# Optimization experiments

Measured on AMD Instinct MI355X. Metric: run time of the kernel, lower is better.

The kernel has to match this reference:

```python
import jax, jax.numpy as jnp
import numpy as np

N, HID, NC, GD, HEADS = 8192, 768, 18, 256, 2
K = 5            # knn_k in the module
E_CLS = 324      # class co-occurrence edges (<= 18*18)
NEG_SLOPE = 0.2  # GATv2Conv default
EPS = 1e-5       # LayerNorm eps


def _ln(x, g, b):
    m = x.mean(-1, keepdims=True)
    v = ((x - m) ** 2).mean(-1, keepdims=True)
    return (x - m) / jnp.sqrt(v + EPS) * g + b


def _seg_softmax(scores, seg, n):
    # softmax over edges grouped by destination node (irregular segments)
    m = jax.ops.segment_max(scores, seg, num_segments=n)
    e = jnp.exp(scores - m[seg])
    s = jax.ops.segment_sum(e, seg, num_segments=n)
    return e / s[seg]


def _gatv2(x, src, dst, wl, bl, wr, br, att, bias, n):
    # PyG GATv2Conv (heads=2, concat=True), eval mode (dropout off)
    xl = (x @ wl.T + bl).reshape(n, HEADS, GD)   # lin_l -> source features
    xr = (x @ wr.T + br).reshape(n, HEADS, GD)   # lin_r -> target features
    h = jax.nn.leaky_relu(xl[src] + xr[dst], NEG_SLOPE)     # [E,H,D]
    scores = jnp.einsum('ehd,hd->eh', h, att)               # [E,H]
    alpha = _seg_softmax(scores, dst, n)
    out = jax.ops.segment_sum(xl[src] * alpha[..., None], dst, num_segments=n)
    return out.reshape(n, HEADS * GD) + bias


def _add_self_loops(src, dst, n):
    # GATv2Conv default add_self_loops=True
    loops = jnp.arange(n)
    return jnp.concatenate([src, loops]), jnp.concatenate([dst, loops])


def _knn_edges(x, k):
    # torch_cluster knn_graph(x, k, loop=True): self-distance 0 is always kept
    x2 = jnp.sum(x * x, -1)
    d = x2[:, None] + x2[None, :] - 2.0 * (x @ x.T)  # [N,N] sq. distances
    _, idx = jax.lax.top_k(-d, k)                    # k nearest incl. self
    src = idx.reshape(-1)                            # neighbors (sources)
    dst = jnp.repeat(jnp.arange(x.shape[0]), k)      # centers (targets)
    return src, dst


def _forward(class_edge_index, instance_features, class_emb,
             gc_wl, gc_bl, gc_wr, gc_br, gc_att, gc_bias,
             gi_wl, gi_bl, gi_wr, gi_br, gi_att, gi_bias,
             q_w, q_b, ctx_w, ctx_b, wv, bv, wo, bo, ln1_g, ln1_b,
             ln2_g, ln2_b, gw_w, gw_b, temperature):
    n = instance_features.shape[0]
    # class graph GATv2
    csrc, cdst = _add_self_loops(class_edge_index[0], class_edge_index[1], NC)
    class_feat = _gatv2(class_emb, csrc, cdst, gc_wl, gc_bl, gc_wr, gc_br,
                        gc_att, gc_bias, NC)                  # [NC, 512]
    # kNN graph + instance GATv2
    isrc, idst = _knn_edges(instance_features, K)
    isrc, idst = _add_self_loops(isrc, idst, n)
    gnn_inst = _gatv2(instance_features, isrc, idst, gi_wl, gi_bl, gi_wr,
                      gi_br, gi_att, gi_bias, n)              # [N, 512]
    ctx = class_feat.mean(0, keepdims=True) + gnn_inst        # [N, 512]
    # cross-attention fusion: q/k/v have seq_len 1, so softmax == 1 and the
    # MHA output reduces to out_proj(v_proj(context_proj(ctx))); query path
    # (q_w, q_b) cancels out of the forward value.
    ctx_p = ctx @ ctx_w.T + ctx_b                             # [N, 768]
    attn = (ctx_p @ wv.T + bv) @ wo.T + bo                    # [N, 768]
    fused = _ln(instance_features + attn, ln1_g, ln1_b)
    # pre_classifier: LayerNorm -> GELU (exact) -> Dropout(eval)
    pre = jax.nn.gelu(_ln(fused, ln2_g, ln2_b), approximate=False)
    # GroupWiseLinear
    logits = jnp.einsum('ch,nh->nc', gw_w[0], pre) + gw_b[0]
    return logits / temperature  # eval-mode temperature scaling


def setup_inputs() -> dict:
    key = jax.random.key(0)
    ks = jax.random.split(key, 32)
    rn = lambda i, shape, s: jax.random.normal(ks[i], shape, jnp.float32) * s
    inp = {
        'instance_features': jax.random.normal(ks[0], (N, HID), jnp.float32),
        'class_edge_index': jax.random.randint(ks[1], (2, E_CLS), 0, NC),
        'class_emb': rn(2, (NC, HID), 0.02),
        'gc_wl': rn(3, (HEADS * GD, HID), 0.02), 'gc_bl': jnp.zeros(HEADS * GD),
        'gc_wr': rn(4, (HEADS * GD, HID), 0.02), 'gc_br': jnp.zeros(HEADS * GD),
        'gc_att': rn(5, (HEADS, GD), 0.1), 'gc_bias': jnp.zeros(HEADS * GD),
        'gi_wl': rn(6, (HEADS * GD, HID), 0.02), 'gi_bl': jnp.zeros(HEADS * GD),
        'gi_wr': rn(7, (HEADS * GD, HID), 0.02), 'gi_br': jnp.zeros(HEADS * GD),
        'gi_att': rn(8, (HEADS, GD), 0.1), 'gi_bias': jnp.zeros(HEADS * GD),
        'q_w': rn(9, (HID, HID), 0.02), 'q_b': jnp.zeros(HID),
        'ctx_w': rn(10, (HID, HEADS * GD), 0.02), 'ctx_b': jnp.zeros(HID),
        'wv': rn(11, (HID, HID), 0.02), 'bv': jnp.zeros(HID),
        'wo': rn(12, (HID, HID), 0.02), 'bo': jnp.zeros(HID),
        'ln1_g': jnp.ones(HID), 'ln1_b': jnp.zeros(HID),
        'ln2_g': jnp.ones(HID), 'ln2_b': jnp.zeros(HID),
        'gw_w': rn(13, (1, NC, HID), 0.036), 'gw_b': jnp.zeros((1, NC)),
        'temperature': jnp.ones(1),
    }
    return inp


def reference(instance_features, class_edge_index, class_emb,
              gc_wl, gc_bl, gc_wr, gc_br, gc_att, gc_bias,
              gi_wl, gi_bl, gi_wr, gi_br, gi_att, gi_bias,
              q_w, q_b, ctx_w, ctx_b, wv, bv, wo, bo, ln1_g, ln1_b,
              ln2_g, ln2_b, gw_w, gw_b, temperature):
    return _forward(class_edge_index, instance_features, class_emb,
                    gc_wl, gc_bl, gc_wr, gc_br, gc_att, gc_bias,
                    gi_wl, gi_bl, gi_wr, gi_br, gi_att, gi_bias,
                    q_w, q_b, ctx_w, ctx_b, wv, bv, wo, bo, ln1_g, ln1_b,
                    ln2_g, ln2_b, gw_w, gw_b, temperature)
```

## Files before the change

kernel.cpp:

```cpp
#include <hip/hip_runtime.h>
#include <hip/hip_bf16.h>
#include <hip/hip_fp16.h>
#include <math.h>

#define NN 8192
#define HIDD 768
#define NCLS 18
#define OD 512
#define ETOT 342
#define NEG 0.2f
#define LN_EPS 1e-5f

typedef __attribute__((ext_vector_type(8))) short bf16x8;
typedef __attribute__((ext_vector_type(4))) float f32x4;

__device__ __forceinline__ void top5_insert(float s, int idx,
    float& d0, float& d1, float& d2, float& d3, float& d4,
    int& i0, int& i1, int& i2, int& i3, int& i4) {
  if (s >= d4) return;
  if (s < d3) {
    d4 = d3; i4 = i3;
    if (s < d2) {
      d3 = d2; i3 = i2;
      if (s < d1) {
        d2 = d1; i2 = i1;
        if (s < d0) { d1 = d0; i1 = i0; d0 = s; i0 = idx; }
        else        { d1 = s;  i1 = idx; }
      } else { d2 = s; i2 = idx; }
    } else { d3 = s; i3 = idx; }
  } else { d4 = s; i4 = idx; }
}

__device__ __forceinline__ void top8k_insert(unsigned key, unsigned (&kk)[8]) {
  if (key >= kk[7]) return;
  int rank = 0;
  #pragma unroll
  for (int k = 0; k < 7; ++k) rank += (key >= kk[k]) ? 1 : 0;
  #pragma unroll
  for (int k = 7; k >= 1; --k) if (k > rank) kk[k] = kk[k-1];
  #pragma unroll
  for (int k = 0; k < 8; ++k) if (k == rank) kk[k] = key;
}

__device__ __forceinline__ void stage16(const void* g, void* l) {
  __builtin_amdgcn_global_load_lds(
      (const __attribute__((address_space(1))) unsigned int*)g,
      (__attribute__((address_space(3))) unsigned int*)l, 16, 0, 0);
}

__device__ __forceinline__ ushort f2b(float v) {
  __hip_bfloat16 b = __float2bfloat16(v);
  return *(ushort*)&b;
}
__device__ __forceinline__ float b2f(ushort u) {
  unsigned uv = ((unsigned)u) << 16;
  return *(float*)&uv;
}

__global__ __launch_bounds__(256) void prep1_kernel(
    const float* __restrict__ X, ushort* __restrict__ Xh, float* __restrict__ x2,
    const float* __restrict__ gi_wl, const float* __restrict__ gi_wr,
    ushort* __restrict__ wlrh,
    const float* __restrict__ cemb, const float* __restrict__ gc_wl,
    const float* __restrict__ gc_bl, const float* __restrict__ gc_wr,
    const float* __restrict__ gc_br, float* __restrict__ xlc, float* __restrict__ xrc,
    const float* __restrict__ wv, const float* __restrict__ ctx_b,
    const float* __restrict__ bv, float* __restrict__ t1b,
    const float* __restrict__ gi_bl, const float* __restrict__ gi_br,
    float* __restrict__ bb) {
  const int bx = blockIdx.x, tid = threadIdx.x;
  if (bx < 2048) {
    const int row = bx * 4 + (tid >> 6);
    const int lane = tid & 63;
    const float4* src = (const float4*)(X + (size_t)row * HIDD);
    ushort4* dst = (ushort4*)(Xh + (size_t)row * HIDD);
    float s = 0.f;
    #pragma unroll
    for (int q = 0; q < 3; ++q) {
      float4 v = src[lane + q * 64];
      s += v.x * v.x + v.y * v.y + v.z * v.z + v.w * v.w;
      dst[lane + q * 64] = make_ushort4(f2b(v.x), f2b(v.y), f2b(v.z), f2b(v.w));
    }
    #pragma unroll
    for (int off = 32; off; off >>= 1) s += __shfl_down(s, off);
    if (lane == 0) x2[row] = s;
  } else if (bx < 2816) {
    int rel = bx - 2048;
    const float* src = gi_wl; ushort* dst = wlrh;
    if (rel >= 384) { rel -= 384; src = gi_wr; dst = wlrh + (size_t)OD * HIDD; }
    const int i = rel * 256 + tid;
    float4 v = ((const float4*)src)[i];
    ((ushort4*)dst)[i] = make_ushort4(f2b(v.x), f2b(v.y), f2b(v.z), f2b(v.w));
  } else if (bx < 2888) {
    int t = (bx - 2816) * 256 + tid;
    const float* W; const float* b; float* Y;
    if (t < NCLS * OD) { W = gc_wl; b = gc_bl; Y = xlc; }
    else { t -= NCLS * OD; W = gc_wr; b = gc_br; Y = xrc; }
    const int row = t / OD, o = t - row * OD;
    const float4* xr4 = (const float4*)(cemb + (size_t)row * HIDD);
    const float4* wr4 = (const float4*)(W + (size_t)o * HIDD);
    float acc = 0.f;
    for (int k = 0; k < HIDD / 4; ++k) {
      const float4 a = xr4[k], w4 = wr4[k];
      acc += a.x * w4.x + a.y * w4.y + a.z * w4.z + a.w * w4.w;
    }
    Y[t] = acc + b[o];
  } else if (bx < 2891) {
    const int t = (bx - 2888) * 256 + tid;
    if (t < HIDD) {
      const float4* cb4 = (const float4*)ctx_b;
      const float4* wv4 = (const float4*)(wv + (size_t)t * HIDD);
      float acc = 0.f;
      for (int k = 0; k < HIDD / 4; ++k) {
        const float4 a = cb4[k], w4 = wv4[k];
        acc += a.x * w4.x + a.y * w4.y + a.z * w4.z + a.w * w4.w;
      }
      t1b[t] = acc + bv[t];
    }
  } else {
    const int t = (bx - 2891) * 256 + tid;
    if (t < OD) bb[t] = gi_bl[t];
    else if (t < 2 * OD) bb[t] = gi_br[t - OD];
  }
}

__global__ __launch_bounds__(256) void gemm_nn_f32(const float* __restrict__ A,
    const float* __restrict__ B, float* __restrict__ Cf, ushort* __restrict__ Ch,
    int M, int N, int K) {
  __shared__ float As[64][33];
  __shared__ float Bs[32][65];
  const int tid = threadIdx.x, tx = tid & 15, ty = tid >> 4;
  const int r0 = blockIdx.x * 64, c0 = blockIdx.y * 64;
  float acc[4][4] = {};
  for (int kt = 0; kt < K; kt += 32) {
    __syncthreads();
    #pragma unroll
    for (int l = 0; l < 8; ++l) {
      const int idx = l * 256 + tid;
      const int m = idx >> 5, k = idx & 31;
      As[m][k] = A[(size_t)(r0 + m) * K + kt + k];
      const int k2 = idx >> 6, n = idx & 63;
      Bs[k2][n] = B[(size_t)(kt + k2) * N + c0 + n];
    }
    __syncthreads();
    #pragma unroll
    for (int k = 0; k < 32; ++k) {
      float a[4], b[4];
      #pragma unroll
      for (int i = 0; i < 4; ++i) a[i] = As[ty * 4 + i][k];
      #pragma unroll
      for (int j = 0; j < 4; ++j) b[j] = Bs[k][tx * 4 + j];
      #pragma unroll
      for (int i = 0; i < 4; ++i)
        #pragma unroll
        for (int j = 0; j < 4; ++j) acc[i][j] += a[i] * b[j];
    }
  }
  #pragma unroll
  for (int i = 0; i < 4; ++i) {
    const int r = r0 + ty * 4 + i;
    #pragma unroll
    for (int j = 0; j < 4; ++j) {
      const int c = c0 + tx * 4 + j;
      if (Ch) Ch[(size_t)r * N + c] = f2b(acc[i][j]);
      else    Cf[(size_t)r * N + c] = acc[i][j];
    }
  }
}

__global__ __launch_bounds__(256) void prep2_kernel(
    const float* __restrict__ wo, const float* __restrict__ t1b,
    const float* __restrict__ bo, float* __restrict__ bp,
    const int* __restrict__ cei, const float* __restrict__ xlc,
    const float* __restrict__ xrc, const float* __restrict__ gc_att,
    const float* __restrict__ gc_bias, float* __restrict__ cmean) {
  __shared__ float sc[ETOT * 2];
  __shared__ int es[ETOT], ed[ETOT];
  __shared__ float mx[NCLS][2], sm[NCLS][2];
  const int bx = blockIdx.x, tid = threadIdx.x;
  if (bx < 3) {
    const int t = bx * 256 + tid;
    if (t < HIDD) {
      const float4* tb4 = (const float4*)t1b;
      const float4* wo4 = (const float4*)(wo + (size_t)t * HIDD);
      float acc = 0.f;
      for (int k = 0; k < HIDD / 4; ++k) {
        const float4 a = tb4[k], w4 = wo4[k];
        acc += a.x * w4.x + a.y * w4.y + a.z * w4.z + a.w * w4.w;
      }
      bp[t] = acc + bo[t];
    }
  } else {
    for (int e = tid; e < ETOT; e += 256) {
      if (e < 324) { es[e] = cei[e]; ed[e] = cei[324 + e]; }
      else         { es[e] = e - 324; ed[e] = e - 324; }
    }
    __syncthreads();
    const int lane = tid & 63, w = tid >> 6;
    for (int t = w; t < ETOT * 2; t += 4) {
      const int e = t >> 1, h = t & 1;
      const float* xlr = xlc + (size_t)es[e] * OD + h * 256;
      const float* xrr = xrc + (size_t)ed[e] * OD + h * 256;
      const float* ar  = gc_att + h * 256;
      float s = 0.f;
      for (int d = lane; d < 256; d += 64) {
        float v = xlr[d] + xrr[d];
        v = v > 0.f ? v : NEG * v;
        s += v * ar[d];
      }
      #pragma unroll
      for (int off = 32; off; off >>= 1) s += __shfl_down(s, off);
      if (lane == 0) sc[t] = s;
    }
    __syncthreads();
    if (tid < NCLS * 2) {
      const int d = tid >> 1, h = tid & 1;
      float m = -3e38f;
      for (int e = 0; e < ETOT; ++e) if (ed[e] == d) m = fmaxf(m, sc[e * 2 + h]);
      float ssum = 0.f;
      for (int e = 0; e < ETOT; ++e) if (ed[e] == d) ssum += expf(sc[e * 2 + h] - m);
      mx[d][h] = m; sm[d][h] = 1.f / ssum;
    }
    __syncthreads();
    for (int t = tid; t < ETOT * 2; t += 256) {
      const int e = t >> 1, h = t & 1;
      sc[t] = expf(sc[t] - mx[ed[e]][h]) * sm[ed[e]][h];
    }
    __syncthreads();
    for (int c = tid; c < OD; c += 256) {
      const int h = c >> 8;
      float acc = 0.f;
      for (int e = 0; e < ETOT; ++e) acc += sc[e * 2 + h] * xlc[(size_t)es[e] * OD + c];
      cmean[c] = acc * (1.f / 18.f) + gc_bias[c];
    }
  }
}

__global__ __launch_bounds__(256, 4) void dist_sym_mfma(
    const ushort* __restrict__ Xh, const float* __restrict__ x2,
    unsigned* __restrict__ pck) {
  __shared__ __align__(16) char lds[32768];
  __shared__ float x2i[128], x2j[128];
  char* const sA = lds;
  char* const sB = lds + 16384;
  __half* const Dh = (__half*)lds;
  unsigned* const ck = (unsigned*)lds;

  const int t = blockIdx.x;
  int by = (int)((sqrtf(8.0f * (float)t + 1.0f) - 1.0f) * 0.5f);
  while ((by + 1) * (by + 2) / 2 <= t) ++by;
  while (by * (by + 1) / 2 > t) --by;
  const int bx = t - by * (by + 1) / 2;

  const int tid = threadIdx.x;
  const int lane = tid & 63, wid = tid >> 6;
  const int fr = lane & 15, fq = lane >> 4;
  const int i0 = bx * 128, j0 = by * 128;
  const int wr = (wid >> 1) * 64, wc = (wid & 1) * 64;
  const bool diag = (bx == by);

  if (tid < 128) x2i[tid] = x2[i0 + tid];
  else x2j[tid - 128] = x2[j0 + tid - 128];

  f32x4 acc[4][4] = {};
  for (int kt = 0; kt < HIDD; kt += 64) {
    __syncthreads();
    #pragma unroll
    for (int q = 0; q < 4; ++q) {
      const int chunkid = q * 256 + tid;
      const int row = chunkid >> 3, cc = chunkid & 7;
      const bf16x8 va = *(const bf16x8*)(Xh + (size_t)(i0 + row) * HIDD + kt + cc * 8);
      const bf16x8 vb = *(const bf16x8*)(Xh + (size_t)(j0 + row) * HIDD + kt + cc * 8);
      const int wi = row * 128 + ((cc ^ (row & 7)) << 4);
      *(bf16x8*)(sA + wi) = va;
      *(bf16x8*)(sB + wi) = vb;
    }
    __syncthreads();
    #pragma unroll
    for (int kk = 0; kk < 2; ++kk) {
      bf16x8 bh[4];
      #pragma unroll
      for (int n = 0; n < 4; ++n) {
        const int br = wc + n * 16 + fr;
        bh[n] = *(const bf16x8*)(sB + br * 128 + (((kk * 4 + fq) ^ (br & 7)) << 4));
      }
      #pragma unroll
      for (int m = 0; m < 4; ++m) {
        const int ar = wr + m * 16 + fr;
        const bf16x8 a = *(const bf16x8*)(sA + ar * 128 + (((kk * 4 + fq) ^ (ar & 7)) << 4));
        #pragma unroll
        for (int n = 0; n < 4; ++n)
          acc[m][n] = __builtin_amdgcn_mfma_f32_16x16x32_bf16(a, bh[n], acc[m][n], 0, 0, 0);
      }
    }
  }
  __syncthreads();
  #pragma unroll
  for (int n = 0; n < 4; ++n) {
    const int col = wc + n * 16 + fr;
    #pragma unroll
    for (int m = 0; m < 4; ++m) {
      #pragma unroll
      for (int j = 0; j < 4; ++j) {
        const int row = wr + m * 16 + fq * 4 + j;
        Dh[row * 128 + ((col + row) & 127)] = __float2half(-2.0f * acc[m][n][j]);
      }
    }
  }
  __syncthreads();

  unsigned ki[8], kj[8];
  #pragma unroll
  for (int k = 0; k < 8; ++k) { ki[k] = 0xFFFFFFFFu; kj[k] = 0xFFFFFFFFu; }
  const int r = tid & 127, h = tid >> 7;
  for (int c = 0; c < 64; ++c) {
    const int col = h * 64 + c;
    const float s = x2j[col] - 768.0f + __half2float(Dh[r * 128 + ((col + r) & 127)]);
    const ushort u = __half_as_ushort(__float2half(s));
    const ushort k16 = (u & 0x8000) ? (ushort)(~u) : (ushort)(u | 0x8000);
    top8k_insert(((unsigned)k16 << 16) | (unsigned)(j0 + col), ki);
  }
  if (!diag) {
    for (int c = 0; c < 64; ++c) {
      const int cr = h * 64 + c;
      const float s = x2i[cr] - 768.0f + __half2float(Dh[cr * 128 + ((r + cr) & 127)]);
      const ushort u = __half_as_ushort(__float2half(s));
      const ushort k16 = (u & 0x8000) ? (ushort)(~u) : (ushort)(u | 0x8000);
      top8k_insert(((unsigned)k16 << 16) | (unsigned)(i0 + cr), kj);
    }
  }
  __syncthreads();
  #pragma unroll
  for (int k = 0; k < 8; ++k) ck[tid * 8 + k] = ki[k];
  __syncthreads();
  if (tid < 128) {
    unsigned mk[8];
    #pragma unroll
    for (int k = 0; k < 8; ++k) mk[k] = ck[tid * 8 + k];
    #pragma unroll
    for (int k = 0; k < 8; ++k) top8k_insert(ck[(tid + 128) * 8 + k], mk);
    const size_t base = ((size_t)(i0 + tid) * 64 + by) * 8;
    #pragma unroll
    for (int k = 0; k < 8; ++k) pck[base + k] = mk[k];
  }
  if (!diag) {
    __syncthreads();
    #pragma unroll
    for (int k = 0; k < 8; ++k) ck[tid * 8 + k] = kj[k];
    __syncthreads();
    if (tid < 128) {
      unsigned mk[8];
      #pragma unroll
      for (int k = 0; k < 8; ++k) mk[k] = ck[tid * 8 + k];
      #pragma unroll
      for (int k = 0; k < 8; ++k) top8k_insert(ck[(tid + 128) * 8 + k], mk);
      const size_t base = ((size_t)(j0 + tid) * 64 + bx) * 8;
      #pragma unroll
      for (int k = 0; k < 8; ++k) pck[base + k] = mk[k];
    }
  }
}

__global__ __launch_bounds__(256) void mr_gat_kernel(
    const float* __restrict__ X, const float* __restrict__ x2,
    const unsigned* __restrict__ pck, const ushort* __restrict__ xlrh,
    const float* __restrict__ att, const float* __restrict__ bias,
    const float* __restrict__ cmean, ushort* __restrict__ ctxh) {
  __shared__ float rows[7][512];
  __shared__ float rsc[8];
  __shared__ int rcand[8];
  __shared__ int nbr[6];
  __shared__ float sc[12];
  __shared__ float alpha[12];
  const int i = blockIdx.x;
  const int tid = threadIdx.x;
  const int lane = tid & 63, w = tid >> 6;

  if (w == 0) {
    unsigned mk[8];
    #pragma unroll
    for (int k = 0; k < 8; ++k) mk[k] = pck[(size_t)i * 512 + lane * 8 + k];
    #pragma unroll
    for (int st = 1; st < 64; st <<= 1) {
      unsigned ok[8];
      #pragma unroll
      for (int k = 0; k < 8; ++k) ok[k] = __shfl_xor(mk[k], st);
      #pragma unroll
      for (int k = 0; k < 8; ++k) top8k_insert(ok[k], mk);
    }
    if (lane < 8) rcand[lane] = (int)(mk[lane] & 0xFFFFu);
  } else {
    const int tt = tid - 64;
    if (tt < 128) {
      const int rr = 5 + (tt >> 6), e4 = tt & 63;
      const bf16x8 v = *(const bf16x8*)(xlrh + (size_t)i * 1024 + (rr == 6 ? 512 : 0) + e4 * 8);
      #pragma unroll
      for (int j = 0; j < 8; ++j) rows[rr][e4 * 8 + j] = b2f((ushort)v[j]);
    }
  }
  __syncthreads();
  {
    const int cnd = w * 2 + (lane >> 5);
    const int sl = lane & 31;
    const int cidx = rcand[cnd];
    const float4* xi = (const float4*)(X + (size_t)i * HIDD);
    const float4* xc = (const float4*)(X + (size_t)cidx * HIDD);
    float acc = 0.f;
    #pragma unroll
    for (int q = 0; q < 6; ++q) {
      const float4 a = xi[sl + q * 32];
      const float4 b = xc[sl + q * 32];
      acc += a.x * b.x + a.y * b.y + a.z * b.z + a.w * b.w;
    }
    #pragma unroll
    for (int off = 16; off; off >>= 1) acc += __shfl_down(acc, off, 32);
    if (sl == 0) rsc[cnd] = x2[cidx] - 2.0f * acc;
  }
  __syncthreads();
  if (tid == 0) {
    float d0 = 3e38f, d1 = 3e38f, d2 = 3e38f, d3 = 3e38f, d4 = 3e38f;
    int i0 = 0, i1 = 0, i2 = 0, i3 = 0, i4 = 0;
    #pragma unroll
    for (int k = 0; k < 8; ++k)
      top5_insert(rsc[k], rcand[k], d0, d1, d2, d3, d4, i0, i1, i2, i3, i4);
    nbr[0] = i0; nbr[1] = i1; nbr[2] = i2; nbr[3] = i3; nbr[4] = i4; nbr[5] = i;
  }
  __syncthreads();
  for (int t2 = tid; t2 < 5 * 64; t2 += 256) {
    const int rr = t2 >> 6, e4 = t2 & 63;
    const bf16x8 v = *(const bf16x8*)(xlrh + (size_t)nbr[rr] * 1024 + e4 * 8);
    #pragma unroll
    for (int j = 0; j < 8; ++j) rows[rr][e4 * 8 + j] = b2f((ushort)v[j]);
  }
  __syncthreads();
  for (int t = w; t < 12; t += 4) {
    const int e = t >> 1, h = t & 1;
    const float* ar = att + h * 256;
    float s = 0.f;
    #pragma unroll
    for (int q = 0; q < 4; ++q) {
      const int d = lane + q * 64;
      float v = rows[e][h * 256 + d] + rows[6][h * 256 + d];
      v = v > 0.f ? v : NEG * v;
      s += v * ar[d];
    }
    #pragma unroll
    for (int off = 32; off; off >>= 1) s += __shfl_down(s, off);
    if (lane == 0) sc[t] = s;
  }
  __syncthreads();
  if (tid < 2) {
    const int h = tid;
    float m = -3e38f;
    #pragma unroll
    for (int e = 0; e < 6; ++e) m = fmaxf(m, sc[e * 2 + h]);
    float ssum = 0.f;
    #pragma unroll
    for (int e = 0; e < 6; ++e) { float ex = expf(sc[e * 2 + h] - m); alpha[e * 2 + h] = ex; ssum += ex; }
    const float inv = 1.f / ssum;
    #pragma unroll
    for (int e = 0; e < 6; ++e) alpha[e * 2 + h] *= inv;
  }
  __syncthreads();
  for (int c = tid; c < OD; c += 256) {
    const int h = c >> 8;
    float acc = 0.f;
    #pragma unroll
    for (int e = 0; e < 6; ++e) acc += alpha[e * 2 + h] * rows[e][c];
    ctxh[(size_t)i * OD + c] = f2b(acc + bias[c] + cmean[c]);
  }
}

__global__ __launch_bounds__(256) void gemm_nt_mfma(const ushort* __restrict__ A,
    const ushort* __restrict__ B, const float* __restrict__ bias,
    float* __restrict__ C, ushort* __restrict__ Cb, int Nc, int K) {
  __shared__ char lds[32768];
  char* const pA = lds;
  char* const pB = lds + 16384;
  const int tid = threadIdx.x;
  const int lane = tid & 63, wid = tid >> 6;
  const int fr = lane & 15, fq = lane >> 4;
  const int r0 = blockIdx.x * 128;
  const int c0 = blockIdx.y * 128;
  const int wr = (wid >> 1) * 64, wc = (wid & 1) * 64;
  f32x4 acc[4][4] = {};
  for (int kt = 0; kt < K; kt += 64) {
    __syncthreads();
    #pragma unroll
    for (int q = 0; q < 4; ++q) {
      const int chunk = wid * 256 + q * 64 + lane;
      const int row = chunk >> 3;
      const int lc = (chunk & 7) ^ (row & 7);
      const int ld = wid * 4096 + q * 1024;
      stage16((const char*)A + ((size_t)(r0 + row) * K + kt) * 2 + (size_t)lc * 16, pA + ld);
      stage16((const char*)B + ((size_t)(c0 + row) * K + kt) * 2 + (size_t)lc * 16, pB + ld);
    }
    __syncthreads();
    #pragma unroll
    for (int kk = 0; kk < 2; ++kk) {
      bf16x8 ah[4], bh[4];
      #pragma unroll
      for (int m = 0; m < 4; ++m) {
        const int ar = wr + m * 16 + fr;
        ah[m] = *(const bf16x8*)(pA + ar * 128 + (((kk * 4 + fq) ^ (ar & 7)) << 4));
      }
      #pragma unroll
      for (int n = 0; n < 4; ++n) {
        const int br = wc + n * 16 + fr;
        bh[n] = *(const bf16x8*)(pB + br * 128 + (((kk * 4 + fq) ^ (br & 7)) << 4));
      }
      #pragma unroll
      for (int m = 0; m < 4; ++m)
        #pragma unroll
        for (int n = 0; n < 4; ++n)
          acc[m][n] = __builtin_amdgcn_mfma_f32_16x16x32_bf16(ah[m], bh[n], acc[m][n], 0, 0, 0);
    }
  }
  #pragma unroll
  for (int n = 0; n < 4; ++n) {
    const int cc = c0 + wc + n * 16 + fr;
    const float bs = bias[cc];
    #pragma unroll
    for (int m = 0; m < 4; ++m) {
      #pragma unroll
      for (int j = 0; j < 4; ++j) {
        const int rr = r0 + wr + m * 16 + fq * 4 + j;
        const float val = acc[m][n][j] + bs;
        if (Cb) Cb[(size_t)rr * Nc + cc] = f2b(val);
        else    C[(size_t)rr * Nc + cc] = val;
      }
    }
  }
}

__global__ __launch_bounds__(256) void epilogue_kernel(const float* __restrict__ inst,
    const float* __restrict__ attn, const float* __restrict__ g1, const float* __restrict__ b1,
    const float* __restrict__ g2, const float* __restrict__ b2, const float* __restrict__ gw,
    const float* __restrict__ gb, const float* __restrict__ temp, float* __restrict__ out) {
  __shared__ float buf[HIDD];
  __shared__ float red[4];
  const int i = blockIdx.x;
  const int tid = threadIdx.x;
  const int lane = tid & 63, w = tid >> 6;
  size_t base = (size_t)i * HIDD;
  float v0 = inst[base + tid]       + attn[base + tid];
  float v1 = inst[base + tid + 256] + attn[base + tid + 256];
  float v2 = inst[base + tid + 512] + attn[base + tid + 512];

  float s = v0 + v1 + v2;
  #pragma unroll
  for (int off = 32; off; off >>= 1) s += __shfl_down(s, off);
  if (lane == 0) red[w] = s;
  __syncthreads();
  float mean = (red[0] + red[1] + red[2] + red[3]) * (1.f / HIDD);
  __syncthreads();
  float e0 = v0 - mean, e1 = v1 - mean, e2 = v2 - mean;
  s = e0 * e0 + e1 * e1 + e2 * e2;
  #pragma unroll
  for (int off = 32; off; off >>= 1) s += __shfl_down(s, off);
  if (lane == 0) red[w] = s;
  __syncthreads();
  float rstd = rsqrtf((red[0] + red[1] + red[2] + red[3]) * (1.f / HIDD) + LN_EPS);
  __syncthreads();
  float y0 = e0 * rstd * g1[tid]       + b1[tid];
  float y1 = e1 * rstd * g1[tid + 256] + b1[tid + 256];
  float y2 = e2 * rstd * g1[tid + 512] + b1[tid + 512];

  s = y0 + y1 + y2;
  #pragma unroll
  for (int off = 32; off; off >>= 1) s += __shfl_down(s, off);
  if (lane == 0) red[w] = s;
  __syncthreads();
  float mean2 = (red[0] + red[1] + red[2] + red[3]) * (1.f / HIDD);
  __syncthreads();
  float f0 = y0 - mean2, f1 = y1 - mean2, f2 = y2 - mean2;
  s = f0 * f0 + f1 * f1 + f2 * f2;
  #pragma unroll
  for (int off = 32; off; off >>= 1) s += __shfl_down(s, off);
  if (lane == 0) red[w] = s;
  __syncthreads();
  float rstd2 = rsqrtf((red[0] + red[1] + red[2] + red[3]) * (1.f / HIDD) + LN_EPS);
  float z0 = f0 * rstd2 * g2[tid]       + b2[tid];
  float z1 = f1 * rstd2 * g2[tid + 256] + b2[tid + 256];
  float z2 = f2 * rstd2 * g2[tid + 512] + b2[tid + 512];
  buf[tid]       = 0.5f * z0 * (1.f + erff(z0 * 0.70710678118654752f));
  buf[tid + 256] = 0.5f * z1 * (1.f + erff(z1 * 0.70710678118654752f));
  buf[tid + 512] = 0.5f * z2 * (1.f + erff(z2 * 0.70710678118654752f));
  __syncthreads();

  float invT = 1.f / temp[0];
  for (int c = w; c < NCLS; c += 4) {
    const float* wr = gw + (size_t)c * HIDD;
    float acc = 0.f;
    for (int d = lane; d < HIDD; d += 64) acc += buf[d] * wr[d];
    #pragma unroll
    for (int off = 32; off; off >>= 1) acc += __shfl_down(acc, off);
    if (lane == 0) out[(size_t)i * NCLS + c] = (acc + gb[c]) * invT;
  }
}

extern "C" void kernel_launch(void* const* d_in, const int* in_sizes, int n_in,
                              void* d_out, int out_size, void* d_ws, size_t ws_size,
                              hipStream_t stream) {
  (void)in_sizes; (void)n_in; (void)out_size; (void)ws_size;
  const float* X       = (const float*)d_in[0];
  const int*   cei     = (const int*)  d_in[1];
  const float* cemb    = (const float*)d_in[2];
  const float* gc_wl   = (const float*)d_in[3];
  const float* gc_bl   = (const float*)d_in[4];
  const float* gc_wr   = (const float*)d_in[5];
  const float* gc_br   = (const float*)d_in[6];
  const float* gc_att  = (const float*)d_in[7];
  const float* gc_bias = (const float*)d_in[8];
  const float* gi_wl   = (const float*)d_in[9];
  const float* gi_bl   = (const float*)d_in[10];
  const float* gi_wr   = (const float*)d_in[11];
  const float* gi_br   = (const float*)d_in[12];
  const float* gi_att  = (const float*)d_in[13];
  const float* gi_bias = (const float*)d_in[14];
  const float* ctx_w   = (const float*)d_in[17];
  const float* ctx_b   = (const float*)d_in[18];
  const float* wv      = (const float*)d_in[19];
  const float* bv      = (const float*)d_in[20];
  const float* wo      = (const float*)d_in[21];
  const float* bo      = (const float*)d_in[22];
  const float* ln1_g   = (const float*)d_in[23];
  const float* ln1_b   = (const float*)d_in[24];
  const float* ln2_g   = (const float*)d_in[25];
  const float* ln2_b   = (const float*)d_in[26];
  const float* gw_w    = (const float*)d_in[27];
  const float* gw_b    = (const float*)d_in[28];
  const float* temp    = (const float*)d_in[29];
  float* out = (float*)d_out;

  float* ws  = (float*)d_ws;
  float* R1  = ws;
  float* R2  = R1 + (size_t)NN * OD;
  float* R3  = R2 + (size_t)NN * OD;
  float* R4  = R3 + (size_t)NN * OD;

  float* x2    = R4;
  ushort* w3h  = (ushort*)(x2 + NN);
  float* t1b   = (float*)(w3h + (size_t)HIDD * OD);
  float* bp    = t1b + HIDD;
  float* bb    = bp + HIDD;
  float* xlc   = bb + 2 * OD;
  float* xrc   = xlc + NCLS * OD;
  float* cmean = xrc + NCLS * OD;

  float* T1     = R1;
  ushort* xlrh  = (ushort*)R1;
  float* attnb  = R1;
  unsigned* pck = (unsigned*)R2;
  ushort* Xh    = (ushort*)R3;
  ushort* wlrh  = (ushort*)(R3 + (size_t)NN * HIDD / 2);
  ushort* ctxh  = (ushort*)R3;

  prep1_kernel<<<2895, 256, 0, stream>>>(X, Xh, x2, gi_wl, gi_wr, wlrh,
      cemb, gc_wl, gc_bl, gc_wr, gc_br, xlc, xrc,
      wv, ctx_b, bv, t1b, gi_bl, gi_br, bb);
  gemm_nn_f32<<<dim3(HIDD / 64, OD / 64), 256, 0, stream>>>(wv, ctx_w, T1, nullptr, HIDD, OD, HIDD);
  gemm_nn_f32<<<dim3(HIDD / 64, OD / 64), 256, 0, stream>>>(wo, T1, nullptr, w3h, HIDD, OD, HIDD);
  prep2_kernel<<<4, 256, 0, stream>>>(wo, t1b, bo, bp, cei, xlc, xrc, gc_att, gc_bias, cmean);
  gemm_nt_mfma<<<dim3(NN / 128, (2 * OD) / 128), 256, 0, stream>>>(Xh, wlrh, bb, nullptr, xlrh, 2 * OD, HIDD);
  dist_sym_mfma<<<2080, 256, 0, stream>>>(Xh, x2, pck);
  mr_gat_kernel<<<NN, 256, 0, stream>>>(X, x2, pck, xlrh, gi_att, gi_bias, cmean, ctxh);
  gemm_nt_mfma<<<dim3(NN / 128, HIDD / 128), 256, 0, stream>>>(ctxh, w3h, bp, attnb, nullptr, HIDD, OD);
  epilogue_kernel<<<NN, 256, 0, stream>>>(X, attnb, ln1_g, ln1_b, ln2_g, ln2_b, gw_w, gw_b, temp, out);
}
```

Baseline: 786.8 us.

## Merge independent prep, GEMM and distance kernels into two multi-role launches

Packs the six launches before the GAT stage into two. The first merged kernel runs the old prep work plus the wv·ctx_w fp32 GEMM. The second runs the symmetric distance/top-k blocks, the xl/xr MFMA GEMM, the wo·T1 GEMM, the bias matvec and the class-graph GAT, all dispatched by block index. The aim is to cut launch gaps and let small, low-occupancy pieces overlap with large ones on idle CUs. T1 moves into its own workspace slot so it no longer aliases xlrh. The cost is shared LDS sized for the largest role and launch bounds that may lower occupancy for the smaller roles.

```diff
diff --git a/kernel.cpp b/kernel.cpp
--- a/kernel.cpp
+++ b/kernel.cpp
@@ -57,7 +57,232 @@
   return *(float*)&uv;
 }
 
-__global__ __launch_bounds__(256) void prep1_kernel(
+__device__ __forceinline__ void gemm_nn_body(const float* __restrict__ A,
+    const float* __restrict__ B, float* __restrict__ Cf, ushort* __restrict__ Ch,
+    int M, int N, int K, int r0, int c0, char* buf, int tid) {
+  float* As = (float*)buf;
+  float* Bs = (float*)(buf + 8448);
+  const int tx = tid & 15, ty = tid >> 4;
+  float acc[4][4] = {};
+  for (int kt = 0; kt < K; kt += 32) {
+    __syncthreads();
+    #pragma unroll
+    for (int l = 0; l < 8; ++l) {
+      const int idx = l * 256 + tid;
+      const int m = idx >> 5, k = idx & 31;
+      As[m * 33 + k] = A[(size_t)(r0 + m) * K + kt + k];
+      const int k2 = idx >> 6, n = idx & 63;
+      Bs[k2 * 65 + n] = B[(size_t)(kt + k2) * N + c0 + n];
+    }
+    __syncthreads();
+    #pragma unroll
+    for (int k = 0; k < 32; ++k) {
+      float a[4], b[4];
+      #pragma unroll
+      for (int i = 0; i < 4; ++i) a[i] = As[(ty * 4 + i) * 33 + k];
+      #pragma unroll
+      for (int j = 0; j < 4; ++j) b[j] = Bs[k * 65 + tx * 4 + j];
+      #pragma unroll
+      for (int i = 0; i < 4; ++i)
+        #pragma unroll
+        for (int j = 0; j < 4; ++j) acc[i][j] += a[i] * b[j];
+    }
+  }
+  #pragma unroll
+  for (int i = 0; i < 4; ++i) {
+    const int r = r0 + ty * 4 + i;
+    #pragma unroll
+    for (int j = 0; j < 4; ++j) {
+      const int c = c0 + tx * 4 + j;
+      if (Ch) Ch[(size_t)r * N + c] = f2b(acc[i][j]);
+      else    Cf[(size_t)r * N + c] = acc[i][j];
+    }
+  }
+}
+
+__device__ __forceinline__ void gemm_nt_body(const ushort* __restrict__ A,
+    const ushort* __restrict__ B, const float* __restrict__ bias,
+    float* __restrict__ C, ushort* __restrict__ Cb, int Nc, int K,
+    int r0, int c0, char* buf, int tid) {
+  char* const pA = buf;
+  char* const pB = buf + 16384;
+  const int lane = tid & 63, wid = tid >> 6;
+  const int fr = lane & 15, fq = lane >> 4;
+  const int wr = (wid >> 1) * 64, wc = (wid & 1) * 64;
+  f32x4 acc[4][4] = {};
+  for (int kt = 0; kt < K; kt += 64) {
+    __syncthreads();
+    #pragma unroll
+    for (int q = 0; q < 4; ++q) {
+      const int chunk = wid * 256 + q * 64 + lane;
+      const int row = chunk >> 3;
+      const int lc = (chunk & 7) ^ (row & 7);
+      const int ld = wid * 4096 + q * 1024;
+      stage16((const char*)A + ((size_t)(r0 + row) * K + kt) * 2 + (size_t)lc * 16, pA + ld);
+      stage16((const char*)B + ((size_t)(c0 + row) * K + kt) * 2 + (size_t)lc * 16, pB + ld);
+    }
+    __syncthreads();
+    #pragma unroll
+    for (int kk = 0; kk < 2; ++kk) {
+      bf16x8 ah[4], bh[4];
+      #pragma unroll
+      for (int m = 0; m < 4; ++m) {
+        const int ar = wr + m * 16 + fr;
+        ah[m] = *(const bf16x8*)(pA + ar * 128 + (((kk * 4 + fq) ^ (ar & 7)) << 4));
+      }
+      #pragma unroll
+      for (int n = 0; n < 4; ++n) {
+        const int br = wc + n * 16 + fr;
+        bh[n] = *(const bf16x8*)(pB + br * 128 + (((kk * 4 + fq) ^ (br & 7)) << 4));
+      }
+      #pragma unroll
+      for (int m = 0; m < 4; ++m)
+        #pragma unroll
+        for (int n = 0; n < 4; ++n)
+          acc[m][n] = __builtin_amdgcn_mfma_f32_16x16x32_bf16(ah[m], bh[n], acc[m][n], 0, 0, 0);
+    }
+  }
+  #pragma unroll
+  for (int n = 0; n < 4; ++n) {
+    const int cc = c0 + wc + n * 16 + fr;
+    const float bs = bias[cc];
+    #pragma unroll
+    for (int m = 0; m < 4; ++m) {
+      #pragma unroll
+      for (int j = 0; j < 4; ++j) {
+        const int rr = r0 + wr + m * 16 + fq * 4 + j;
+        const float val = acc[m][n][j] + bs;
+        if (Cb) Cb[(size_t)rr * Nc + cc] = f2b(val);
+        else    C[(size_t)rr * Nc + cc] = val;
+      }
+    }
+  }
+}
+
+__device__ __forceinline__ void dist_body(int t, int tid,
+    const ushort* __restrict__ Xh, const float* __restrict__ x2,
+    unsigned* __restrict__ pck, char* buf) {
+  char* const sA = buf;
+  char* const sB = buf + 16384;
+  __half* const Dh = (__half*)buf;
+  unsigned* const ck = (unsigned*)buf;
+  float* const x2i = (float*)(buf + 32768);
+  float* const x2j = x2i + 128;
+
+  int by = (int)((sqrtf(8.0f * (float)t + 1.0f) - 1.0f) * 0.5f);
+  while ((by + 1) * (by + 2) / 2 <= t) ++by;
+  while (by * (by + 1) / 2 > t) --by;
+  const int bx = t - by * (by + 1) / 2;
+
+  const int lane = tid & 63, wid = tid >> 6;
+  const int fr = lane & 15, fq = lane >> 4;
+  const int i0 = bx * 128, j0 = by * 128;
+  const int wr = (wid >> 1) * 64, wc = (wid & 1) * 64;
+  const bool diag = (bx == by);
+
+  if (tid < 128) x2i[tid] = x2[i0 + tid];
+  else x2j[tid - 128] = x2[j0 + tid - 128];
+
+  f32x4 acc[4][4] = {};
+  for (int kt = 0; kt < HIDD; kt += 64) {
+    __syncthreads();
+    #pragma unroll
+    for (int q = 0; q < 4; ++q) {
+      const int chunkid = q * 256 + tid;
+      const int row = chunkid >> 3, cc = chunkid & 7;
+      const bf16x8 va = *(const bf16x8*)(Xh + (size_t)(i0 + row) * HIDD + kt + cc * 8);
+      const bf16x8 vb = *(const bf16x8*)(Xh + (size_t)(j0 + row) * HIDD + kt + cc * 8);
+      const int wi = row * 128 + ((cc ^ (row & 7)) << 4);
+      *(bf16x8*)(sA + wi) = va;
+      *(bf16x8*)(sB + wi) = vb;
+    }
+    __syncthreads();
+    #pragma unroll
+    for (int kk = 0; kk < 2; ++kk) {
+      bf16x8 bh[4];
+      #pragma unroll
+      for (int n = 0; n < 4; ++n) {
+        const int br = wc + n * 16 + fr;
+        bh[n] = *(const bf16x8*)(sB + br * 128 + (((kk * 4 + fq) ^ (br & 7)) << 4));
+      }
+      #pragma unroll
+      for (int m = 0; m < 4; ++m) {
+        const int ar = wr + m * 16 + fr;
+        const bf16x8 a = *(const bf16x8*)(sA + ar * 128 + (((kk * 4 + fq) ^ (ar & 7)) << 4));
+        #pragma unroll
+        for (int n = 0; n < 4; ++n)
+          acc[m][n] = __builtin_amdgcn_mfma_f32_16x16x32_bf16(a, bh[n], acc[m][n], 0, 0, 0);
+      }
+    }
+  }
+  __syncthreads();
+  #pragma unroll
+  for (int n = 0; n < 4; ++n) {
+    const int col = wc + n * 16 + fr;
+    #pragma unroll
+    for (int m = 0; m < 4; ++m) {
+      #pragma unroll
+      for (int j = 0; j < 4; ++j) {
+        const int row = wr + m * 16 + fq * 4 + j;
+        Dh[row * 128 + ((col + row) & 127)] = __float2half(-2.0f * acc[m][n][j]);
+      }
+    }
+  }
+  __syncthreads();
+
+  unsigned ki[8], kj[8];
+  #pragma unroll
+  for (int k = 0; k < 8; ++k) { ki[k] = 0xFFFFFFFFu; kj[k] = 0xFFFFFFFFu; }
+  const int r = tid & 127, h = tid >> 7;
+  for (int c = 0; c < 64; ++c) {
+    const int col = h * 64 + c;
+    const float s = x2j[col] - 768.0f + __half2float(Dh[r * 128 + ((col + r) & 127)]);
+    const ushort u = __half_as_ushort(__float2half(s));
+    const ushort k16 = (u & 0x8000) ? (ushort)(~u) : (ushort)(u | 0x8000);
+    top8k_insert(((unsigned)k16 << 16) | (unsigned)(j0 + col), ki);
+  }
+  if (!diag) {
+    for (int c = 0; c < 64; ++c) {
+      const int cr = h * 64 + c;
+      const float s = x2i[cr] - 768.0f + __half2float(Dh[cr * 128 + ((r + cr) & 127)]);
+      const ushort u = __half_as_ushort(__float2half(s));
+      const ushort k16 = (u & 0x8000) ? (ushort)(~u) : (ushort)(u | 0x8000);
+      top8k_insert(((unsigned)k16 << 16) | (unsigned)(i0 + cr), kj);
+    }
+  }
+  __syncthreads();
+  #pragma unroll
+  for (int k = 0; k < 8; ++k) ck[tid * 8 + k] = ki[k];
+  __syncthreads();
+  if (tid < 128) {
+    unsigned mk[8];
+    #pragma unroll
+    for (int k = 0; k < 8; ++k) mk[k] = ck[tid * 8 + k];
+    #pragma unroll
+    for (int k = 0; k < 8; ++k) top8k_insert(ck[(tid + 128) * 8 + k], mk);
+    const size_t base = ((size_t)(i0 + tid) * 64 + by) * 8;
+    #pragma unroll
+    for (int k = 0; k < 8; ++k) pck[base + k] = mk[k];
+  }
+  if (!diag) {
+    __syncthreads();
+    #pragma unroll
+    for (int k = 0; k < 8; ++k) ck[tid * 8 + k] = kj[k];
+    __syncthreads();
+    if (tid < 128) {
+      unsigned mk[8];
+      #pragma unroll
+      for (int k = 0; k < 8; ++k) mk[k] = ck[tid * 8 + k];
+      #pragma unroll
+      for (int k = 0; k < 8; ++k) top8k_insert(ck[(tid + 128) * 8 + k], mk);
+      const size_t base = ((size_t)(j0 + tid) * 64 + bx) * 8;
+      #pragma unroll
+      for (int k = 0; k < 8; ++k) pck[base + k] = mk[k];
+    }
+  }
+}
+
+__global__ __launch_bounds__(256) void fused1_kernel(
     const float* __restrict__ X, ushort* __restrict__ Xh, float* __restrict__ x2,
     const float* __restrict__ gi_wl, const float* __restrict__ gi_wr,
     ushort* __restrict__ wlrh,
@@ -67,7 +292,8 @@
     const float* __restrict__ wv, const float* __restrict__ ctx_b,
     const float* __restrict__ bv, float* __restrict__ t1b,
     const float* __restrict__ gi_bl, const float* __restrict__ gi_br,
-    float* __restrict__ bb) {
+    float* __restrict__ bb, const float* __restrict__ ctx_w, float* __restrict__ T1) {
+  __shared__ __align__(16) char buf[16768];
   const int bx = blockIdx.x, tid = threadIdx.x;
   if (bx < 2048) {
     const int row = bx * 4 + (tid >> 6);
@@ -117,69 +343,43 @@
       }
       t1b[t] = acc + bv[t];
     }
-  } else {
+  } else if (bx < 2895) {
     const int t = (bx - 2891) * 256 + tid;
     if (t < OD) bb[t] = gi_bl[t];
     else if (t < 2 * OD) bb[t] = gi_br[t - OD];
-  }
-}
-
-__global__ __launch_bounds__(256) void gemm_nn_f32(const float* __restrict__ A,
-    const float* __restrict__ B, float* __restrict__ Cf, ushort* __restrict__ Ch,
-    int M, int N, int K) {
-  __shared__ float As[64][33];
-  __shared__ float Bs[32][65];
-  const int tid = threadIdx.x, tx = tid & 15, ty = tid >> 4;
-  const int r0 = blockIdx.x * 64, c0 = blockIdx.y * 64;
-  float acc[4][4] = {};
-  for (int kt = 0; kt < K; kt += 32) {
-    __syncthreads();
-    #pragma unroll
-    for (int l = 0; l < 8; ++l) {
-      const int idx = l * 256 + tid;
-      const int m = idx >> 5, k = idx & 31;
-      As[m][k] = A[(size_t)(r0 + m) * K + kt + k];
-      const int k2 = idx >> 6, n = idx & 63;
-      Bs[k2][n] = B[(size_t)(kt + k2) * N + c0 + n];
-    }
-    __syncthreads();
-    #pragma unroll
-    for (int k = 0; k < 32; ++k) {
-      float a[4], b[4];
-      #pragma unroll
-      for (int i = 0; i < 4; ++i) a[i] = As[ty * 4 + i][k];
-      #pragma unroll
-      for (int j = 0; j < 4; ++j) b[j] = Bs[k][tx * 4 + j];
-      #pragma unroll
-      for (int i = 0; i < 4; ++i)
-        #pragma unroll
-        for (int j = 0; j < 4; ++j) acc[i][j] += a[i] * b[j];
-    }
-  }
-  #pragma unroll
-  for (int i = 0; i < 4; ++i) {
-    const int r = r0 + ty * 4 + i;
-    #pragma unroll
-    for (int j = 0; j < 4; ++j) {
-      const int c = c0 + tx * 4 + j;
-      if (Ch) Ch[(size_t)r * N + c] = f2b(acc[i][j]);
-      else    Cf[(size_t)r * N + c] = acc[i][j];
-    }
-  }
-}
-
-__global__ __launch_bounds__(256) void prep2_kernel(
-    const float* __restrict__ wo, const float* __restrict__ t1b,
-    const float* __restrict__ bo, float* __restrict__ bp,
-    const int* __restrict__ cei, const float* __restrict__ xlc,
-    const float* __restrict__ xrc, const float* __restrict__ gc_att,
-    const float* __restrict__ gc_bias, float* __restrict__ cmean) {
-  __shared__ float sc[ETOT * 2];
-  __shared__ int es[ETOT], ed[ETOT];
-  __shared__ float mx[NCLS][2], sm[NCLS][2];
-  const int bx = blockIdx.x, tid = threadIdx.x;
-  if (bx < 3) {
-    const int t = bx * 256 + tid;
+  } else {
+    const int rel = bx - 2895;
+    gemm_nn_body(wv, ctx_w, T1, nullptr, HIDD, OD, HIDD,
+                 (rel >> 3) * 64, (rel & 7) * 64, buf, tid);
+  }
+}
+
+__global__ __launch_bounds__(256, 4) void fused2_kernel(
+    const ushort* __restrict__ Xh, const float* __restrict__ x2,
+    unsigned* __restrict__ pck,
+    const ushort* __restrict__ wlrh, const float* __restrict__ bb,
+    ushort* __restrict__ xlrh,
+    const float* __restrict__ wo, const float* __restrict__ T1,
+    ushort* __restrict__ w3h,
+    const float* __restrict__ t1b, const float* __restrict__ bo,
+    float* __restrict__ bp, const int* __restrict__ cei,
+    const float* __restrict__ xlc, const float* __restrict__ xrc,
+    const float* __restrict__ gc_att, const float* __restrict__ gc_bias,
+    float* __restrict__ cmean) {
+  __shared__ __align__(16) char buf[33792];
+  const int bid = blockIdx.x, tid = threadIdx.x;
+  if (bid < 2080) {
+    dist_body(bid, tid, Xh, x2, pck, buf);
+  } else if (bid < 2592) {
+    const int rel = bid - 2080;
+    gemm_nt_body(Xh, wlrh, bb, nullptr, xlrh, 2 * OD, HIDD,
+                 (rel >> 3) * 128, (rel & 7) * 128, buf, tid);
+  } else if (bid < 2688) {
+    const int rel = bid - 2592;
+    gemm_nn_body(wo, T1, nullptr, w3h, HIDD, OD, HIDD,
+                 (rel >> 3) * 64, (rel & 7) * 64, buf, tid);
+  } else if (bid < 2691) {
+    const int t = (bid - 2688) * 256 + tid;
     if (t < HIDD) {
       const float4* tb4 = (const float4*)t1b;
       const float4* wo4 = (const float4*)(wo + (size_t)t * HIDD);
@@ -191,6 +391,11 @@
       bp[t] = acc + bo[t];
     }
   } else {
+    float* sc = (float*)buf;
+    int* es = (int*)(buf + 2736);
+    int* ed = es + ETOT;
+    float* mx = (float*)(buf + 2736 + 2736);
+    float* sm = mx + NCLS * 2;
     for (int e = tid; e < ETOT; e += 256) {
       if (e < 324) { es[e] = cei[e]; ed[e] = cei[324 + e]; }
       else         { es[e] = e - 324; ed[e] = e - 324; }
@@ -219,12 +424,12 @@
       for (int e = 0; e < ETOT; ++e) if (ed[e] == d) m = fmaxf(m, sc[e * 2 + h]);
       float ssum = 0.f;
       for (int e = 0; e < ETOT; ++e) if (ed[e] == d) ssum += expf(sc[e * 2 + h] - m);
-      mx[d][h] = m; sm[d][h] = 1.f / ssum;
+      mx[d * 2 + h] = m; sm[d * 2 + h] = 1.f / ssum;
     }
     __syncthreads();
     for (int t = tid; t < ETOT * 2; t += 256) {
       const int e = t >> 1, h = t & 1;
-      sc[t] = expf(sc[t] - mx[ed[e]][h]) * sm[ed[e]][h];
+      sc[t] = expf(sc[t] - mx[ed[e] * 2 + h]) * sm[ed[e] * 2 + h];
     }
     __syncthreads();
     for (int c = tid; c < OD; c += 256) {
@@ -232,131 +437,6 @@
       float acc = 0.f;
       for (int e = 0; e < ETOT; ++e) acc += sc[e * 2 + h] * xlc[(size_t)es[e] * OD + c];
       cmean[c] = acc * (1.f / 18.f) + gc_bias[c];
-    }
-  }
-}
-
-__global__ __launch_bounds__(256, 4) void dist_sym_mfma(
-    const ushort* __restrict__ Xh, const float* __restrict__ x2,
-    unsigned* __restrict__ pck) {
-  __shared__ __align__(16) char lds[32768];
-  __shared__ float x2i[128], x2j[128];
-  char* const sA = lds;
-  char* const sB = lds + 16384;
-  __half* const Dh = (__half*)lds;
-  unsigned* const ck = (unsigned*)lds;
-
-  const int t = blockIdx.x;
-  int by = (int)((sqrtf(8.0f * (float)t + 1.0f) - 1.0f) * 0.5f);
-  while ((by + 1) * (by + 2) / 2 <= t) ++by;
-  while (by * (by + 1) / 2 > t) --by;
-  const int bx = t - by * (by + 1) / 2;
-
-  const int tid = threadIdx.x;
-  const int lane = tid & 63, wid = tid >> 6;
-  const int fr = lane & 15, fq = lane >> 4;
-  const int i0 = bx * 128, j0 = by * 128;
-  const int wr = (wid >> 1) * 64, wc = (wid & 1) * 64;
-  const bool diag = (bx == by);
-
-  if (tid < 128) x2i[tid] = x2[i0 + tid];
-  else x2j[tid - 128] = x2[j0 + tid - 128];
-
-  f32x4 acc[4][4] = {};
-  for (int kt = 0; kt < HIDD; kt += 64) {
-    __syncthreads();
-    #pragma unroll
-    for (int q = 0; q < 4; ++q) {
-      const int chunkid = q * 256 + tid;
-      const int row = chunkid >> 3, cc = chunkid & 7;
-      const bf16x8 va = *(const bf16x8*)(Xh + (size_t)(i0 + row) * HIDD + kt + cc * 8);
-      const bf16x8 vb = *(const bf16x8*)(Xh + (size_t)(j0 + row) * HIDD + kt + cc * 8);
-      const int wi = row * 128 + ((cc ^ (row & 7)) << 4);
-      *(bf16x8*)(sA + wi) = va;
-      *(bf16x8*)(sB + wi) = vb;
-    }
-    __syncthreads();
-    #pragma unroll
-    for (int kk = 0; kk < 2; ++kk) {
-      bf16x8 bh[4];
-      #pragma unroll
-      for (int n = 0; n < 4; ++n) {
-        const int br = wc + n * 16 + fr;
-        bh[n] = *(const bf16x8*)(sB + br * 128 + (((kk * 4 + fq) ^ (br & 7)) << 4));
-      }
-      #pragma unroll
-      for (int m = 0; m < 4; ++m) {
-        const int ar = wr + m * 16 + fr;
-        const bf16x8 a = *(const bf16x8*)(sA + ar * 128 + (((kk * 4 + fq) ^ (ar & 7)) << 4));
-        #pragma unroll
-        for (int n = 0; n < 4; ++n)
-          acc[m][n] = __builtin_amdgcn_mfma_f32_16x16x32_bf16(a, bh[n], acc[m][n], 0, 0, 0);
-      }
-    }
-  }
-  __syncthreads();
-  #pragma unroll
-  for (int n = 0; n < 4; ++n) {
-    const int col = wc + n * 16 + fr;
-    #pragma unroll
-    for (int m = 0; m < 4; ++m) {
-      #pragma unroll
-      for (int j = 0; j < 4; ++j) {
-        const int row = wr + m * 16 + fq * 4 + j;
-        Dh[row * 128 + ((col + row) & 127)] = __float2half(-2.0f * acc[m][n][j]);
-      }
-    }
-  }
-  __syncthreads();
-
-  unsigned ki[8], kj[8];
-  #pragma unroll
-  for (int k = 0; k < 8; ++k) { ki[k] = 0xFFFFFFFFu; kj[k] = 0xFFFFFFFFu; }
-  const int r = tid & 127, h = tid >> 7;
-  for (int c = 0; c < 64; ++c) {
-    const int col = h * 64 + c;
-    const float s = x2j[col] - 768.0f + __half2float(Dh[r * 128 + ((col + r) & 127)]);
-    const ushort u = __half_as_ushort(__float2half(s));
-    const ushort k16 = (u & 0x8000) ? (ushort)(~u) : (ushort)(u | 0x8000);
-    top8k_insert(((unsigned)k16 << 16) | (unsigned)(j0 + col), ki);
-  }
-  if (!diag) {
-    for (int c = 0; c < 64; ++c) {
-      const int cr = h * 64 + c;
-      const float s = x2i[cr] - 768.0f + __half2float(Dh[cr * 128 + ((r + cr) & 127)]);
-      const ushort u = __half_as_ushort(__float2half(s));
-      const ushort k16 = (u & 0x8000) ? (ushort)(~u) : (ushort)(u | 0x8000);
-      top8k_insert(((unsigned)k16 << 16) | (unsigned)(i0 + cr), kj);
-    }
-  }
-  __syncthreads();
-  #pragma unroll
-  for (int k = 0; k < 8; ++k) ck[tid * 8 + k] = ki[k];
-  __syncthreads();
-  if (tid < 128) {
-    unsigned mk[8];
-    #pragma unroll
-    for (int k = 0; k < 8; ++k) mk[k] = ck[tid * 8 + k];
-    #pragma unroll
-    for (int k = 0; k < 8; ++k) top8k_insert(ck[(tid + 128) * 8 + k], mk);
-    const size_t base = ((size_t)(i0 + tid) * 64 + by) * 8;
-    #pragma unroll
-    for (int k = 0; k < 8; ++k) pck[base + k] = mk[k];
-  }
-  if (!diag) {
-    __syncthreads();
-    #pragma unroll
-    for (int k = 0; k < 8; ++k) ck[tid * 8 + k] = kj[k];
-    __syncthreads();
-    if (tid < 128) {
-      unsigned mk[8];
-      #pragma unroll
-      for (int k = 0; k < 8; ++k) mk[k] = ck[tid * 8 + k];
-      #pragma unroll
-      for (int k = 0; k < 8; ++k) top8k_insert(ck[(tid + 128) * 8 + k], mk);
-      const size_t base = ((size_t)(j0 + tid) * 64 + bx) * 8;
-      #pragma unroll
-      for (int k = 0; k < 8; ++k) pck[base + k] = mk[k];
     }
   }
 }
@@ -474,63 +554,9 @@
 __global__ __launch_bounds__(256) void gemm_nt_mfma(const ushort* __restrict__ A,
     const ushort* __restrict__ B, const float* __restrict__ bias,
     float* __restrict__ C, ushort* __restrict__ Cb, int Nc, int K) {
-  __shared__ char lds[32768];
-  char* const pA = lds;
-  char* const pB = lds + 16384;
-  const int tid = threadIdx.x;
-  const int lane = tid & 63, wid = tid >> 6;
-  const int fr = lane & 15, fq = lane >> 4;
-  const int r0 = blockIdx.x * 128;
-  const int c0 = blockIdx.y * 128;
-  const int wr = (wid >> 1) * 64, wc = (wid & 1) * 64;
-  f32x4 acc[4][4] = {};
-  for (int kt = 0; kt < K; kt += 64) {
-    __syncthreads();
-    #pragma unroll
-    for (int q = 0; q < 4; ++q) {
-      const int chunk = wid * 256 + q * 64 + lane;
-      const int row = chunk >> 3;
-      const int lc = (chunk & 7) ^ (row & 7);
-      const int ld = wid * 4096 + q * 1024;
-      stage16((const char*)A + ((size_t)(r0 + row) * K + kt) * 2 + (size_t)lc * 16, pA + ld);
-      stage16((const char*)B + ((size_t)(c0 + row) * K + kt) * 2 + (size_t)lc * 16, pB + ld);
-    }
-    __syncthreads();
-    #pragma unroll
-    for (int kk = 0; kk < 2; ++kk) {
-      bf16x8 ah[4], bh[4];
-      #pragma unroll
-      for (int m = 0; m < 4; ++m) {
-        const int ar = wr + m * 16 + fr;
-        ah[m] = *(const bf16x8*)(pA + ar * 128 + (((kk * 4 + fq) ^ (ar & 7)) << 4));
-      }
-      #pragma unroll
-      for (int n = 0; n < 4; ++n) {
-        const int br = wc + n * 16 + fr;
-        bh[n] = *(const bf16x8*)(pB + br * 128 + (((kk * 4 + fq) ^ (br & 7)) << 4));
-      }
-      #pragma unroll
-      for (int m = 0; m < 4; ++m)
-        #pragma unroll
-        for (int n = 0; n < 4; ++n)
-          acc[m][n] = __builtin_amdgcn_mfma_f32_16x16x32_bf16(ah[m], bh[n], acc[m][n], 0, 0, 0);
-    }
-  }
-  #pragma unroll
-  for (int n = 0; n < 4; ++n) {
-    const int cc = c0 + wc + n * 16 + fr;
-    const float bs = bias[cc];
-    #pragma unroll
-    for (int m = 0; m < 4; ++m) {
-      #pragma unroll
-      for (int j = 0; j < 4; ++j) {
-        const int rr = r0 + wr + m * 16 + fq * 4 + j;
-        const float val = acc[m][n][j] + bs;
-        if (Cb) Cb[(size_t)rr * Nc + cc] = f2b(val);
-        else    C[(size_t)rr * Nc + cc] = val;
-      }
-    }
-  }
+  __shared__ __align__(16) char lds[32768];
+  gemm_nt_body(A, B, bias, C, Cb, Nc, K, blockIdx.x * 128, blockIdx.y * 128,
+               lds, threadIdx.x);
 }
 
 __global__ __launch_bounds__(256) void epilogue_kernel(const float* __restrict__ inst,
@@ -647,8 +673,8 @@
   float* xlc   = bb + 2 * OD;
   float* xrc   = xlc + NCLS * OD;
   float* cmean = xrc + NCLS * OD;
-
-  float* T1     = R1;
+  float* T1    = cmean + OD;
+
   ushort* xlrh  = (ushort*)R1;
   float* attnb  = R1;
   unsigned* pck = (unsigned*)R2;
@@ -656,14 +682,11 @@
   ushort* wlrh  = (ushort*)(R3 + (size_t)NN * HIDD / 2);
   ushort* ctxh  = (ushort*)R3;
 
-  prep1_kernel<<<2895, 256, 0, stream>>>(X, Xh, x2, gi_wl, gi_wr, wlrh,
+  fused1_kernel<<<2991, 256, 0, stream>>>(X, Xh, x2, gi_wl, gi_wr, wlrh,
       cemb, gc_wl, gc_bl, gc_wr, gc_br, xlc, xrc,
-      wv, ctx_b, bv, t1b, gi_bl, gi_br, bb);
-  gemm_nn_f32<<<dim3(HIDD / 64, OD / 64), 256, 0, stream>>>(wv, ctx_w, T1, nullptr, HIDD, OD, HIDD);
-  gemm_nn_f32<<<dim3(HIDD / 64, OD / 64), 256, 0, stream>>>(wo, T1, nullptr, w3h, HIDD, OD, HIDD);
-  prep2_kernel<<<4, 256, 0, stream>>>(wo, t1b, bo, bp, cei, xlc, xrc, gc_att, gc_bias, cmean);
-  gemm_nt_mfma<<<dim3(NN / 128, (2 * OD) / 128), 256, 0, stream>>>(Xh, wlrh, bb, nullptr, xlrh, 2 * OD, HIDD);
-  dist_sym_mfma<<<2080, 256, 0, stream>>>(Xh, x2, pck);
+      wv, ctx_b, bv, t1b, gi_bl, gi_br, bb, ctx_w, T1);
+  fused2_kernel<<<2692, 256, 0, stream>>>(Xh, x2, pck, wlrh, bb, xlrh,
+      wo, T1, w3h, t1b, bo, bp, cei, xlc, xrc, gc_att, gc_bias, cmean);
   mr_gat_kernel<<<NN, 256, 0, stream>>>(X, x2, pck, xlrh, gi_att, gi_bias, cmean, ctxh);
   gemm_nt_mfma<<<dim3(NN / 128, HIDD / 128), 256, 0, stream>>>(ctxh, w3h, bp, attnb, nullptr, HIDD, OD);
   epilogue_kernel<<<NN, 256, 0, stream>>>(X, attnb, ln1_g, ln1_b, ln2_g, ln2_b, gw_w, gw_b, temp, out);
```

Measured after the change: 630.3 us. -19.9%, faster.
